# Optimization experiments

Hardware: AMD Instinct MI355X
Metric: run time of the kernel (lower is better)

The kernel has to match this reference:

```python
import jax, jax.numpy as jnp
import numpy as np

N_SEQ, MAX_LEN, H_DIM, N_CHAR = 8, 4096, 1024, 256


def setup_inputs() -> dict:
    key = jax.random.key(0)
    ks = jax.random.split(key, 10)
    n_char_ev = 32768
    L, E = 12, 16384
    char_i_seq = jax.random.randint(ks[0], (n_char_ev,), 0, N_SEQ)
    char_i_pos = jax.random.randint(ks[1], (n_char_ev,), 0, MAX_LEN)
    char_ids = jax.random.randint(ks[2], (n_char_ev,), 0, N_CHAR)
    grp_i_seq = jax.random.randint(ks[3], (L, E), 0, N_SEQ)
    grp_i_first = jax.random.randint(ks[4], (L, E), 0, MAX_LEN)
    grp_i_second = jax.random.randint(ks[5], (L, E), 0, MAX_LEN)
    grp_i_pos = jax.random.randint(ks[6], (L, E), 0, MAX_LEN)
    # Learned params: embedding table (std = 1/sqrt(h_dim)) and composer Linear(2h -> h)
    emb_char = jax.random.normal(ks[7], (N_CHAR, H_DIM), dtype=jnp.float32) * (1.0 / H_DIM ** 0.5)
    W = jax.random.normal(ks[8], (2 * H_DIM, H_DIM), dtype=jnp.float32) * (1.0 / (2 * H_DIM) ** 0.5)
    b = jnp.zeros((H_DIM,), dtype=jnp.float32)
    return {"char_i_seq": char_i_seq, "char_i_pos": char_i_pos, "char_ids": char_ids,
            "grp_i_seq": grp_i_seq, "grp_i_first": grp_i_first, "grp_i_second": grp_i_second,
            "grp_i_pos": grp_i_pos, "emb_char": emb_char, "W": W, "b": b}


def reference(char_i_seq, char_i_pos, char_ids, grp_i_seq, grp_i_first,
              grp_i_second, grp_i_pos, emb_char, W, b):
    # h_frag: [n_seq, max_len, h_dim]
    h = jnp.zeros((N_SEQ, MAX_LEN, H_DIM), dtype=emb_char.dtype)
    # Leaf characters: embedding lookup + scatter-add
    h = h.at[char_i_seq, char_i_pos].add(emb_char[char_ids])

    def composer(left, right):
        # tanh(Linear(concat(left, right))) : [E, 2h] @ [2h, h] -> [E, h]
        return jnp.tanh(jnp.concatenate([left, right], axis=-1) @ W + b)

    def level_step(h, idx):
        i_seq, i_first, i_second, i_pos = idx
        out = composer(h[i_seq, i_first], h[i_seq, i_second])  # gather -> compose
        return h.at[i_seq, i_pos].add(out), None                # scatter-add

    h, _ = jax.lax.scan(level_step, h, (grp_i_seq, grp_i_first, grp_i_second, grp_i_pos))
    h = h.at[:, 0].set(0.0)  # h_frag[:, 0].fill_(0)
    return h
```

## Files before the change

### kernel.cpp

```cpp
#include <hip/hip_runtime.h>

#define NS 8
#define ML 4096
#define HD 1024
#define K2 2048
#define NEV 32768
#define NLEV 12
#define NE 16384
#define NSLOT (NS * ML)
#define CAP 8
#define BK 64
#define NT (K2 / BK)
#define LDS_BYTES 131072

typedef __attribute__((ext_vector_type(8))) short bf16x8;
typedef __attribute__((ext_vector_type(4))) float f32x4;

typedef __attribute__((address_space(1))) const void cvoid_g;
typedef __attribute__((address_space(3))) void void_l;

static __device__ __forceinline__ void load_lds_16(const void* g, void* l) {
    __builtin_amdgcn_global_load_lds((cvoid_g*)g, (void_l*)l, 16, 0, 0);
}

static __device__ __forceinline__ unsigned short f2bf(float f) {
    unsigned u = __float_as_uint(f);
    unsigned r = (u + 0x7fffu + ((u >> 16) & 1u)) >> 16;
    return (unsigned short)r;
}

static __device__ __forceinline__ float fast_tanh(float x) {
    return 1.0f - 2.0f / (__expf(2.0f * x) + 1.0f);
}

__global__ void wt_kernel(const float* __restrict__ W, unsigned short* __restrict__ WbT) {
    __shared__ unsigned short tile[64][65];
    const int t = threadIdx.x;
    const int k0 = blockIdx.x * 64;
    const int n0 = blockIdx.y * 64;
#pragma unroll
    for (int i = 0; i < 16; i++) {
        int idx = i * 256 + t;
        int r = idx >> 6, c = idx & 63;
        tile[r][c] = f2bf(W[(size_t)(k0 + r) * HD + n0 + c]);
    }
    __syncthreads();
#pragma unroll
    for (int i = 0; i < 16; i++) {
        int idx = i * 256 + t;
        int r = idx >> 6, c = idx & 63;
        WbT[(size_t)(n0 + r) * K2 + k0 + c] = tile[c][r];
    }
}

__global__ void char_ticket(const int* __restrict__ cseq, const int* __restrict__ cpos,
                            int* __restrict__ counts, int* __restrict__ ticket,
                            int* __restrict__ evlist) {
    const int e = blockIdx.x * 256 + threadIdx.x;
    if (e >= NEV) return;
    const int slot = cseq[e] * ML + cpos[e];
    const int t = atomicAdd(&counts[slot], 1);
    ticket[e] = t;
    if (t < CAP) evlist[slot * CAP + t] = e;
}

__global__ void char_slot_sum(const int* __restrict__ counts, const int* __restrict__ evlist,
                              const int* __restrict__ cid, const float* __restrict__ emb,
                              float* __restrict__ h) {
    const int slot = blockIdx.x;
    const int t = threadIdx.x;
    int n = counts[slot];
    if (n > CAP) n = CAP;
    float4 acc = {0.f, 0.f, 0.f, 0.f};
    for (int i = 0; i < n; i++) {
        const int e = evlist[slot * CAP + i];
        const int id = cid[e];
        const float4 v = ((const float4*)(emb + (size_t)id * HD))[t];
        acc.x += v.x; acc.y += v.y; acc.z += v.z; acc.w += v.w;
    }
    ((float4*)(h + (size_t)slot * HD))[t] = acc;
}

__global__ void char_overflow(const int* __restrict__ cseq, const int* __restrict__ cpos,
                              const int* __restrict__ cid, const int* __restrict__ ticket,
                              const float* __restrict__ emb, float* __restrict__ h) {
    const int e0 = blockIdx.x * 128;
    const int t = threadIdx.x;
    for (int i = 0; i < 128; i++) {
        const int e = e0 + i;
        if (ticket[e] < CAP) continue;
        const int slot = cseq[e] * ML + cpos[e];
        const int id = cid[e];
        const float4 v = ((const float4*)(emb + (size_t)id * HD))[t];
        float* dst = h + (size_t)slot * HD + t * 4;
        atomicAdd(dst + 0, v.x);
        atomicAdd(dst + 1, v.y);
        atomicAdd(dst + 2, v.z);
        atomicAdd(dst + 3, v.w);
    }
}

__global__ void grp_count(const int* __restrict__ iseq, const int* __restrict__ ipos,
                          int* __restrict__ gcounts) {
    const int idx = blockIdx.x * 256 + threadIdx.x;
    if (idx >= NLEV * NE) return;
    const int lev = idx >> 14;
    atomicAdd(&gcounts[lev * NSLOT + iseq[idx] * ML + ipos[idx]], 1);
}

__global__ void grp_dup(const int* __restrict__ iseq, const int* __restrict__ ipos,
                        const int* __restrict__ gcounts, unsigned char* __restrict__ dup) {
    const int idx = blockIdx.x * 256 + threadIdx.x;
    if (idx >= NLEV * NE) return;
    const int lev = idx >> 14;
    dup[idx] = (gcounts[lev * NSLOT + iseq[idx] * ML + ipos[idx]] > 1) ? 1 : 0;
}

__global__ void gather_x(const float* __restrict__ h, const int* __restrict__ iseq,
                         const int* __restrict__ ifirst, const int* __restrict__ isecond,
                         unsigned short* __restrict__ X) {
    const int e = blockIdx.x;
    const int t = threadIdx.x;
    const int seq = iseq[e], f = ifirst[e], s = isecond[e];
    const float4 a = ((const float4*)(h + ((size_t)seq * ML + f) * HD))[t];
    const float4 b = ((const float4*)(h + ((size_t)seq * ML + s) * HD))[t];
    ushort4 pa, pb;
    pa.x = f2bf(a.x); pa.y = f2bf(a.y); pa.z = f2bf(a.z); pa.w = f2bf(a.w);
    pb.x = f2bf(b.x); pb.y = f2bf(b.y); pb.z = f2bf(b.z); pb.w = f2bf(b.w);
    *(ushort4*)(X + (size_t)e * K2 + t * 4) = pa;
    *(ushort4*)(X + (size_t)e * K2 + HD + t * 4) = pb;
}

__global__ __launch_bounds__(512, 2) void gemm_scatter(
    const unsigned short* __restrict__ X,
    const unsigned short* __restrict__ WbT,
    const float* __restrict__ bias,
    const int* __restrict__ iseq, const int* __restrict__ ipos,
    const unsigned char* __restrict__ dup,
    float* __restrict__ h) {
    extern __shared__ unsigned short lds[];
    const int t = threadIdx.x;
    const int lane = t & 63;
    const int w = t >> 6;
    const int wm = w >> 2;
    const int wn = (w & 3) * 64;
    const int fr = lane & 15, fq = lane >> 4;

    const int bid = blockIdx.x;
    const int xcd = bid & 7, bix = bid >> 3;
    const int row0 = ((xcd & 1) * 32 + bix) * 256;
    const int col0 = (xcd >> 1) * 256;

    const int tr = t >> 3;
    const int sp = (t & 7) ^ (tr & 7);
    const unsigned short* Asrc = X + (size_t)(row0 + tr) * K2 + sp * 8;
    const unsigned short* Bsrc = WbT + (size_t)(col0 + tr) * K2 + sp * 8;

    f32x4 acc[8][4];
#pragma unroll
    for (int i = 0; i < 8; i++)
#pragma unroll
        for (int j = 0; j < 4; j++) acc[i][j] = (f32x4){0.f, 0.f, 0.f, 0.f};

    {
        unsigned short* dA = lds;
        unsigned short* dB = lds + 16384;
        load_lds_16(Bsrc + (size_t)(0 * 64) * K2, &dB[(0 * 512 + t) * 8]);
        load_lds_16(Bsrc + (size_t)(1 * 64) * K2, &dB[(1 * 512 + t) * 8]);
        load_lds_16(Bsrc + (size_t)(2 * 64) * K2, &dB[(2 * 512 + t) * 8]);
        load_lds_16(Bsrc + (size_t)(3 * 64) * K2, &dB[(3 * 512 + t) * 8]);
        load_lds_16(Asrc + (size_t)(0 * 64) * K2, &dA[(0 * 512 + t) * 8]);
        load_lds_16(Asrc + (size_t)(2 * 64) * K2, &dA[(2 * 512 + t) * 8]);
        load_lds_16(Asrc + (size_t)(1 * 64) * K2, &dA[(1 * 512 + t) * 8]);
        load_lds_16(Asrc + (size_t)(3 * 64) * K2, &dA[(3 * 512 + t) * 8]);
        asm volatile("s_waitcnt vmcnt(2)" ::: "memory");
    }
    __builtin_amdgcn_s_barrier();
    asm volatile("" ::: "memory");

    for (int kt = 0; kt < NT; kt++) {
        const int d = kt & 1;
        const unsigned short* sA = lds + d * 32768;
        const unsigned short* sB = sA + 16384;
        unsigned short* nA = lds + (d ^ 1) * 32768;
        unsigned short* nB = nA + 16384;
        const size_t ko = (size_t)(kt + 1) * BK;
        const bool st = (kt + 1 < NT);

        bf16x8 af0[2][4], af1[2][4], bf0[2][2], bf1[2][2];

#pragma unroll
        for (int ks = 0; ks < 2; ks++) {
            const int qs = ((ks * 4 + fq) ^ (fr & 7)) * 8;
#pragma unroll
            for (int mt = 0; mt < 4; mt++)
                af0[ks][mt] = *(const bf16x8*)&sA[(wm * 128 + mt * 16 + fr) * BK + qs];
#pragma unroll
            for (int nt = 0; nt < 2; nt++)
                bf0[ks][nt] = *(const bf16x8*)&sB[(wn + nt * 16 + fr) * BK + qs];
        }
        if (st) {
            load_lds_16(Bsrc + (size_t)(0 * 64) * K2 + ko, &nB[(0 * 512 + t) * 8]);
            load_lds_16(Bsrc + (size_t)(1 * 64) * K2 + ko, &nB[(1 * 512 + t) * 8]);
        }
        asm volatile("" ::: "memory");
        __builtin_amdgcn_s_barrier();
        asm volatile("" ::: "memory");
        __builtin_amdgcn_s_setprio(1);
#pragma unroll
        for (int ks = 0; ks < 2; ks++)
#pragma unroll
            for (int mt = 0; mt < 4; mt++)
#pragma unroll
                for (int nt = 0; nt < 2; nt++)
                    acc[mt][nt] = __builtin_amdgcn_mfma_f32_16x16x32_bf16(
                        af0[ks][mt], bf0[ks][nt], acc[mt][nt], 0, 0, 0);
        __builtin_amdgcn_s_setprio(0);
        asm volatile("" ::: "memory");
        __builtin_amdgcn_s_barrier();
        asm volatile("" ::: "memory");

#pragma unroll
        for (int ks = 0; ks < 2; ks++) {
            const int qs = ((ks * 4 + fq) ^ (fr & 7)) * 8;
#pragma unroll
            for (int nt = 0; nt < 2; nt++)
                bf1[ks][nt] = *(const bf16x8*)&sB[(wn + 32 + nt * 16 + fr) * BK + qs];
        }
        if (st) {
            load_lds_16(Bsrc + (size_t)(2 * 64) * K2 + ko, &nB[(2 * 512 + t) * 8]);
            load_lds_16(Bsrc + (size_t)(3 * 64) * K2 + ko, &nB[(3 * 512 + t) * 8]);
        }
        asm volatile("" ::: "memory");
        __builtin_amdgcn_s_barrier();
        asm volatile("" ::: "memory");
        __builtin_amdgcn_s_setprio(1);
#pragma unroll
        for (int ks = 0; ks < 2; ks++)
#pragma unroll
            for (int mt = 0; mt < 4; mt++)
#pragma unroll
                for (int nt = 0; nt < 2; nt++)
                    acc[mt][2 + nt] = __builtin_amdgcn_mfma_f32_16x16x32_bf16(
                        af0[ks][mt], bf1[ks][nt], acc[mt][2 + nt], 0, 0, 0);
        __builtin_amdgcn_s_setprio(0);
        if (st) { asm volatile("s_waitcnt vmcnt(4)" ::: "memory"); }
        else    { asm volatile("s_waitcnt vmcnt(0)" ::: "memory"); }
        __builtin_amdgcn_s_barrier();
        asm volatile("" ::: "memory");

#pragma unroll
        for (int ks = 0; ks < 2; ks++) {
            const int qs = ((ks * 4 + fq) ^ (fr & 7)) * 8;
#pragma unroll
            for (int mt = 0; mt < 4; mt++)
                af1[ks][mt] = *(const bf16x8*)&sA[(wm * 128 + 64 + mt * 16 + fr) * BK + qs];
        }
        if (st) {
            load_lds_16(Asrc + (size_t)(0 * 64) * K2 + ko, &nA[(0 * 512 + t) * 8]);
            load_lds_16(Asrc + (size_t)(2 * 64) * K2 + ko, &nA[(2 * 512 + t) * 8]);
        }
        asm volatile("" ::: "memory");
        __builtin_amdgcn_s_barrier();
        asm volatile("" ::: "memory");
        __builtin_amdgcn_s_setprio(1);
#pragma unroll
        for (int ks = 0; ks < 2; ks++)
#pragma unroll
            for (int mt = 0; mt < 4; mt++)
#pragma unroll
                for (int nt = 0; nt < 2; nt++)
                    acc[4 + mt][nt] = __builtin_amdgcn_mfma_f32_16x16x32_bf16(
                        af1[ks][mt], bf0[ks][nt], acc[4 + mt][nt], 0, 0, 0);
        __builtin_amdgcn_s_setprio(0);
        asm volatile("" ::: "memory");
        __builtin_amdgcn_s_barrier();
        asm volatile("" ::: "memory");

        if (st) {
            load_lds_16(Asrc + (size_t)(1 * 64) * K2 + ko, &nA[(1 * 512 + t) * 8]);
            load_lds_16(Asrc + (size_t)(3 * 64) * K2 + ko, &nA[(3 * 512 + t) * 8]);
        }
        asm volatile("" ::: "memory");
        __builtin_amdgcn_s_setprio(1);
#pragma unroll
        for (int ks = 0; ks < 2; ks++)
#pragma unroll
            for (int mt = 0; mt < 4; mt++)
#pragma unroll
                for (int nt = 0; nt < 2; nt++)
                    acc[4 + mt][2 + nt] = __builtin_amdgcn_mfma_f32_16x16x32_bf16(
                        af1[ks][mt], bf1[ks][nt], acc[4 + mt][2 + nt], 0, 0, 0);
        __builtin_amdgcn_s_setprio(0);
        if (st) { asm volatile("s_waitcnt vmcnt(2)" ::: "memory"); }
        else    { asm volatile("s_waitcnt vmcnt(0)" ::: "memory"); }
        __builtin_amdgcn_s_barrier();
        asm volatile("" ::: "memory");
    }

    float bv[4];
#pragma unroll
    for (int ni = 0; ni < 4; ni++) bv[ni] = bias[col0 + wn + ni * 16 + fr];
#pragma unroll
    for (int mi = 0; mi < 8; mi++) {
#pragma unroll
        for (int r = 0; r < 4; r++) {
            const int e = row0 + wm * 128 + mi * 16 + fq * 4 + r;
            const int seq = iseq[e], pos = ipos[e];
            float* hrow = h + ((size_t)seq * ML + pos) * HD + col0 + wn;
            if (dup[e]) {
#pragma unroll
                for (int ni = 0; ni < 4; ni++) {
                    float x = fast_tanh(acc[mi][ni][r] + bv[ni]);
                    atomicAdd(&hrow[ni * 16 + fr], x);
                }
            } else {
#pragma unroll
                for (int ni = 0; ni < 4; ni++) {
                    float x = fast_tanh(acc[mi][ni][r] + bv[ni]);
                    hrow[ni * 16 + fr] += x;
                }
            }
        }
    }
}

__global__ void zero_first(float* __restrict__ h) {
    const int t = blockIdx.x * 256 + threadIdx.x;
    const int seq = t >> 10, d = t & 1023;
    h[(size_t)seq * ML * HD + d] = 0.0f;
}

extern "C" void kernel_launch(void* const* d_in, const int* in_sizes, int n_in,
                              void* d_out, int out_size, void* d_ws, size_t ws_size,
                              hipStream_t stream) {
    const int* char_i_seq = (const int*)d_in[0];
    const int* char_i_pos = (const int*)d_in[1];
    const int* char_ids   = (const int*)d_in[2];
    const int* grp_i_seq    = (const int*)d_in[3];
    const int* grp_i_first  = (const int*)d_in[4];
    const int* grp_i_second = (const int*)d_in[5];
    const int* grp_i_pos    = (const int*)d_in[6];
    const float* emb = (const float*)d_in[7];
    const float* W   = (const float*)d_in[8];
    const float* b   = (const float*)d_in[9];
    float* h = (float*)d_out;

    unsigned short* WbT = (unsigned short*)d_ws;
    unsigned short* X   = (unsigned short*)((char*)d_ws + (8u << 20));
    int* counts = (int*)((char*)d_ws + (72u << 20));
    int* ticket = (int*)((char*)d_ws + (72u << 20) + (1u << 18));
    int* evlist = (int*)((char*)d_ws + (72u << 20) + (1u << 19));
    int* gcounts = (int*)((char*)d_ws + (74u << 20));
    unsigned char* gdup = (unsigned char*)((char*)d_ws + (76u << 20));

    static bool attr_done = false;
    if (!attr_done) {
        (void)hipFuncSetAttribute((const void*)gemm_scatter,
                                  hipFuncAttributeMaxDynamicSharedMemorySize, LDS_BYTES);
        attr_done = true;
    }

    hipMemsetAsync(counts, 0, NSLOT * sizeof(int), stream);
    hipMemsetAsync(gcounts, 0, (size_t)NLEV * NSLOT * sizeof(int), stream);
    wt_kernel<<<dim3(32, 16), 256, 0, stream>>>(W, WbT);
    char_ticket<<<NEV / 256, 256, 0, stream>>>(char_i_seq, char_i_pos, counts, ticket, evlist);
    char_slot_sum<<<NSLOT, 256, 0, stream>>>(counts, evlist, char_ids, emb, h);
    char_overflow<<<NEV / 128, 256, 0, stream>>>(char_i_seq, char_i_pos, char_ids, ticket, emb, h);
    grp_count<<<(NLEV * NE) / 256, 256, 0, stream>>>(grp_i_seq, grp_i_pos, gcounts);
    grp_dup<<<(NLEV * NE) / 256, 256, 0, stream>>>(grp_i_seq, grp_i_pos, gcounts, gdup);

    for (int lev = 0; lev < NLEV; lev++) {
        const int* iseq = grp_i_seq + lev * NE;
        const int* ifir = grp_i_first + lev * NE;
        const int* isec = grp_i_second + lev * NE;
        const int* ipos = grp_i_pos + lev * NE;
        gather_x<<<NE, 256, 0, stream>>>(h, iseq, ifir, isec, X);
        gemm_scatter<<<dim3(256), 512, LDS_BYTES, stream>>>(X, WbT, b, iseq, ipos,
                                                            gdup + lev * NE, h);
    }
    zero_first<<<32, 256, 0, stream>>>(h);
}
```

Measured before the change: 1.511 ms.

## Gather GEMM A-operand directly from persistent bf16 mirror of h

Keeps a bf16 copy of the whole h tensor, initialised once and then refreshed per level only at the rows just scattered to. The GEMM now loads its A tiles straight from that mirror using per-row first/second offsets, so the per-level gather kernel that built the materialised X buffer goes away. Barriers are also merged with waitcnts into single inline asm statements. The cost is a full-tensor bf16 conversion up front (64 MB of fp32 read) and a refresh pass each level, and the per-row gathered loads inside the GEMM are less regular than the old contiguous X rows.

```diff
diff --git a/kernel.cpp b/kernel.cpp
--- a/kernel.cpp
+++ b/kernel.cpp
@@ -116,26 +116,31 @@
     dup[idx] = (gcounts[lev * NSLOT + iseq[idx] * ML + ipos[idx]] > 1) ? 1 : 0;
 }
 
-__global__ void gather_x(const float* __restrict__ h, const int* __restrict__ iseq,
-                         const int* __restrict__ ifirst, const int* __restrict__ isecond,
-                         unsigned short* __restrict__ X) {
+__global__ void hbf_init(const float* __restrict__ h, unsigned short* __restrict__ hbf) {
+    const size_t i = (size_t)blockIdx.x * 256 + threadIdx.x;
+    const float4 v = ((const float4*)h)[i];
+    ushort4 p;
+    p.x = f2bf(v.x); p.y = f2bf(v.y); p.z = f2bf(v.z); p.w = f2bf(v.w);
+    ((ushort4*)hbf)[i] = p;
+}
+
+__global__ void hbf_refresh(const float* __restrict__ h, const int* __restrict__ iseq,
+                            const int* __restrict__ ipos, unsigned short* __restrict__ hbf) {
     const int e = blockIdx.x;
     const int t = threadIdx.x;
-    const int seq = iseq[e], f = ifirst[e], s = isecond[e];
-    const float4 a = ((const float4*)(h + ((size_t)seq * ML + f) * HD))[t];
-    const float4 b = ((const float4*)(h + ((size_t)seq * ML + s) * HD))[t];
-    ushort4 pa, pb;
-    pa.x = f2bf(a.x); pa.y = f2bf(a.y); pa.z = f2bf(a.z); pa.w = f2bf(a.w);
-    pb.x = f2bf(b.x); pb.y = f2bf(b.y); pb.z = f2bf(b.z); pb.w = f2bf(b.w);
-    *(ushort4*)(X + (size_t)e * K2 + t * 4) = pa;
-    *(ushort4*)(X + (size_t)e * K2 + HD + t * 4) = pb;
+    const size_t row = (size_t)iseq[e] * ML + ipos[e];
+    const float4 v = ((const float4*)(h + row * HD))[t];
+    ushort4 p;
+    p.x = f2bf(v.x); p.y = f2bf(v.y); p.z = f2bf(v.z); p.w = f2bf(v.w);
+    ((ushort4*)(hbf + row * HD))[t] = p;
 }
 
 __global__ __launch_bounds__(512, 2) void gemm_scatter(
-    const unsigned short* __restrict__ X,
+    const unsigned short* __restrict__ hbf,
     const unsigned short* __restrict__ WbT,
     const float* __restrict__ bias,
-    const int* __restrict__ iseq, const int* __restrict__ ipos,
+    const int* __restrict__ iseq, const int* __restrict__ ifirst,
+    const int* __restrict__ isecond, const int* __restrict__ ipos,
     const unsigned char* __restrict__ dup,
     float* __restrict__ h) {
     extern __shared__ unsigned short lds[];
@@ -153,7 +158,14 @@
 
     const int tr = t >> 3;
     const int sp = (t & 7) ^ (tr & 7);
-    const unsigned short* Asrc = X + (size_t)(row0 + tr) * K2 + sp * 8;
+    unsigned offA0[4], offA1[4];
+#pragma unroll
+    for (int c = 0; c < 4; c++) {
+        const int e = row0 + tr + c * 64;
+        const int seq = iseq[e];
+        offA0[c] = (unsigned)((seq * ML + ifirst[e]) * HD + sp * 8);
+        offA1[c] = (unsigned)((seq * ML + isecond[e]) * HD + sp * 8);
+    }
     const unsigned short* Bsrc = WbT + (size_t)(col0 + tr) * K2 + sp * 8;
 
     f32x4 acc[8][4];
@@ -169,14 +181,12 @@
         load_lds_16(Bsrc + (size_t)(1 * 64) * K2, &dB[(1 * 512 + t) * 8]);
         load_lds_16(Bsrc + (size_t)(2 * 64) * K2, &dB[(2 * 512 + t) * 8]);
         load_lds_16(Bsrc + (size_t)(3 * 64) * K2, &dB[(3 * 512 + t) * 8]);
-        load_lds_16(Asrc + (size_t)(0 * 64) * K2, &dA[(0 * 512 + t) * 8]);
-        load_lds_16(Asrc + (size_t)(2 * 64) * K2, &dA[(2 * 512 + t) * 8]);
-        load_lds_16(Asrc + (size_t)(1 * 64) * K2, &dA[(1 * 512 + t) * 8]);
-        load_lds_16(Asrc + (size_t)(3 * 64) * K2, &dA[(3 * 512 + t) * 8]);
-        asm volatile("s_waitcnt vmcnt(2)" ::: "memory");
-    }
-    __builtin_amdgcn_s_barrier();
-    asm volatile("" ::: "memory");
+        load_lds_16(hbf + offA0[0], &dA[(0 * 512 + t) * 8]);
+        load_lds_16(hbf + offA0[2], &dA[(2 * 512 + t) * 8]);
+        load_lds_16(hbf + offA0[1], &dA[(1 * 512 + t) * 8]);
+        load_lds_16(hbf + offA0[3], &dA[(3 * 512 + t) * 8]);
+    }
+    asm volatile("s_waitcnt vmcnt(2)\n\ts_barrier" ::: "memory");
 
     for (int kt = 0; kt < NT; kt++) {
         const int d = kt & 1;
@@ -185,6 +195,8 @@
         unsigned short* nA = lds + (d ^ 1) * 32768;
         unsigned short* nB = nA + 16384;
         const size_t ko = (size_t)(kt + 1) * BK;
+        const unsigned koA = (unsigned)(((kt + 1) * BK) & 1023);
+        const int hsel = (kt + 1) >= (NT / 2);
         const bool st = (kt + 1 < NT);
 
         bf16x8 af0[2][4], af1[2][4], bf0[2][2], bf1[2][2];
@@ -203,9 +215,7 @@
             load_lds_16(Bsrc + (size_t)(0 * 64) * K2 + ko, &nB[(0 * 512 + t) * 8]);
             load_lds_16(Bsrc + (size_t)(1 * 64) * K2 + ko, &nB[(1 * 512 + t) * 8]);
         }
-        asm volatile("" ::: "memory");
-        __builtin_amdgcn_s_barrier();
-        asm volatile("" ::: "memory");
+        asm volatile("s_barrier" ::: "memory");
         __builtin_amdgcn_s_setprio(1);
 #pragma unroll
         for (int ks = 0; ks < 2; ks++)
@@ -216,9 +226,7 @@
                     acc[mt][nt] = __builtin_amdgcn_mfma_f32_16x16x32_bf16(
                         af0[ks][mt], bf0[ks][nt], acc[mt][nt], 0, 0, 0);
         __builtin_amdgcn_s_setprio(0);
-        asm volatile("" ::: "memory");
-        __builtin_amdgcn_s_barrier();
-        asm volatile("" ::: "memory");
+        asm volatile("s_barrier" ::: "memory");
 
 #pragma unroll
         for (int ks = 0; ks < 2; ks++) {
@@ -231,9 +239,7 @@
             load_lds_16(Bsrc + (size_t)(2 * 64) * K2 + ko, &nB[(2 * 512 + t) * 8]);
             load_lds_16(Bsrc + (size_t)(3 * 64) * K2 + ko, &nB[(3 * 512 + t) * 8]);
         }
-        asm volatile("" ::: "memory");
-        __builtin_amdgcn_s_barrier();
-        asm volatile("" ::: "memory");
+        asm volatile("s_barrier" ::: "memory");
         __builtin_amdgcn_s_setprio(1);
 #pragma unroll
         for (int ks = 0; ks < 2; ks++)
@@ -244,10 +250,8 @@
                     acc[mt][2 + nt] = __builtin_amdgcn_mfma_f32_16x16x32_bf16(
                         af0[ks][mt], bf1[ks][nt], acc[mt][2 + nt], 0, 0, 0);
         __builtin_amdgcn_s_setprio(0);
-        if (st) { asm volatile("s_waitcnt vmcnt(4)" ::: "memory"); }
-        else    { asm volatile("s_waitcnt vmcnt(0)" ::: "memory"); }
-        __builtin_amdgcn_s_barrier();
-        asm volatile("" ::: "memory");
+        if (st) { asm volatile("s_waitcnt vmcnt(4)\n\ts_barrier" ::: "memory"); }
+        else    { asm volatile("s_waitcnt vmcnt(0)\n\ts_barrier" ::: "memory"); }
 
 #pragma unroll
         for (int ks = 0; ks < 2; ks++) {
@@ -257,12 +261,12 @@
                 af1[ks][mt] = *(const bf16x8*)&sA[(wm * 128 + 64 + mt * 16 + fr) * BK + qs];
         }
         if (st) {
-            load_lds_16(Asrc + (size_t)(0 * 64) * K2 + ko, &nA[(0 * 512 + t) * 8]);
-            load_lds_16(Asrc + (size_t)(2 * 64) * K2 + ko, &nA[(2 * 512 + t) * 8]);
-        }
-        asm volatile("" ::: "memory");
-        __builtin_amdgcn_s_barrier();
-        asm volatile("" ::: "memory");
+            const unsigned o0 = (hsel ? offA1[0] : offA0[0]) + koA;
+            const unsigned o2 = (hsel ? offA1[2] : offA0[2]) + koA;
+            load_lds_16(hbf + o0, &nA[(0 * 512 + t) * 8]);
+            load_lds_16(hbf + o2, &nA[(2 * 512 + t) * 8]);
+        }
+        asm volatile("s_barrier" ::: "memory");
         __builtin_amdgcn_s_setprio(1);
 #pragma unroll
         for (int ks = 0; ks < 2; ks++)
@@ -273,15 +277,14 @@
                     acc[4 + mt][nt] = __builtin_amdgcn_mfma_f32_16x16x32_bf16(
                         af1[ks][mt], bf0[ks][nt], acc[4 + mt][nt], 0, 0, 0);
         __builtin_amdgcn_s_setprio(0);
-        asm volatile("" ::: "memory");
-        __builtin_amdgcn_s_barrier();
-        asm volatile("" ::: "memory");
+        asm volatile("s_barrier" ::: "memory");
 
         if (st) {
-            load_lds_16(Asrc + (size_t)(1 * 64) * K2 + ko, &nA[(1 * 512 + t) * 8]);
-            load_lds_16(Asrc + (size_t)(3 * 64) * K2 + ko, &nA[(3 * 512 + t) * 8]);
-        }
-        asm volatile("" ::: "memory");
+            const unsigned o1 = (hsel ? offA1[1] : offA0[1]) + koA;
+            const unsigned o3 = (hsel ? offA1[3] : offA0[3]) + koA;
+            load_lds_16(hbf + o1, &nA[(1 * 512 + t) * 8]);
+            load_lds_16(hbf + o3, &nA[(3 * 512 + t) * 8]);
+        }
         __builtin_amdgcn_s_setprio(1);
 #pragma unroll
         for (int ks = 0; ks < 2; ks++)
@@ -292,10 +295,8 @@
                     acc[4 + mt][2 + nt] = __builtin_amdgcn_mfma_f32_16x16x32_bf16(
                         af1[ks][mt], bf1[ks][nt], acc[4 + mt][2 + nt], 0, 0, 0);
         __builtin_amdgcn_s_setprio(0);
-        if (st) { asm volatile("s_waitcnt vmcnt(2)" ::: "memory"); }
-        else    { asm volatile("s_waitcnt vmcnt(0)" ::: "memory"); }
-        __builtin_amdgcn_s_barrier();
-        asm volatile("" ::: "memory");
+        if (st) { asm volatile("s_waitcnt vmcnt(2)\n\ts_barrier" ::: "memory"); }
+        else    { asm volatile("s_waitcnt vmcnt(0)\n\ts_barrier" ::: "memory"); }
     }
 
     float bv[4];
@@ -347,7 +348,7 @@
     float* h = (float*)d_out;
 
     unsigned short* WbT = (unsigned short*)d_ws;
-    unsigned short* X   = (unsigned short*)((char*)d_ws + (8u << 20));
+    unsigned short* hbf = (unsigned short*)((char*)d_ws + (8u << 20));
     int* counts = (int*)((char*)d_ws + (72u << 20));
     int* ticket = (int*)((char*)d_ws + (72u << 20) + (1u << 18));
     int* evlist = (int*)((char*)d_ws + (72u << 20) + (1u << 19));
@@ -369,15 +370,17 @@
     char_overflow<<<NEV / 128, 256, 0, stream>>>(char_i_seq, char_i_pos, char_ids, ticket, emb, h);
     grp_count<<<(NLEV * NE) / 256, 256, 0, stream>>>(grp_i_seq, grp_i_pos, gcounts);
     grp_dup<<<(NLEV * NE) / 256, 256, 0, stream>>>(grp_i_seq, grp_i_pos, gcounts, gdup);
+    hbf_init<<<NSLOT, 256, 0, stream>>>(h, hbf);
 
     for (int lev = 0; lev < NLEV; lev++) {
         const int* iseq = grp_i_seq + lev * NE;
         const int* ifir = grp_i_first + lev * NE;
         const int* isec = grp_i_second + lev * NE;
         const int* ipos = grp_i_pos + lev * NE;
-        gather_x<<<NE, 256, 0, stream>>>(h, iseq, ifir, isec, X);
-        gemm_scatter<<<dim3(256), 512, LDS_BYTES, stream>>>(X, WbT, b, iseq, ipos,
-                                                            gdup + lev * NE, h);
+        gemm_scatter<<<dim3(256), 512, LDS_BYTES, stream>>>(hbf, WbT, b, iseq, ifir, isec,
+                                                            ipos, gdup + lev * NE, h);
+        if (lev + 1 < NLEV)
+            hbf_refresh<<<NE, 256, 0, stream>>>(h, iseq, ipos, hbf);
     }
     zero_first<<<32, 256, 0, stream>>>(h);
 }
```

Result: faster. 1.415 ms (-6.4%).
